# Kernel tuning notes

Measured on AMD Instinct MI355X. Metric: run time of the kernel, lower is better.

Reference implementation:

```python
import jax, jax.numpy as jnp
import numpy as np
from jax import lax

DN = ('NCDHW', 'OIDHW', 'NCDHW')


def dwconv(x, w, b):
    # depthwise 3D conv, 'same' padding (groups == channels of this branch)
    k = w.shape[-1]
    p = k // 2
    y = lax.conv_general_dilated(x, w, (1, 1, 1), [(p, p)] * 3,
                                 dimension_numbers=DN,
                                 feature_group_count=x.shape[1])
    return y + b[None, :, None, None, None]


def group_norm(x, w, b, groups=4, eps=1e-5):
    B, C, D, H, W = x.shape
    xr = x.reshape(B, groups, C // groups, D, H, W)
    mu = xr.mean(axis=(2, 3, 4, 5), keepdims=True)
    var = xr.var(axis=(2, 3, 4, 5), keepdims=True)
    xn = ((xr - mu) / jnp.sqrt(var + eps)).reshape(B, C, D, H, W)
    return xn * w[None, :, None, None, None] + b[None, :, None, None, None]


def instance_norm(x, eps=1e-5):
    # torch InstanceNorm3d default: affine=False, biased var, per (n,c) over spatial
    mu = x.mean(axis=(2, 3, 4), keepdims=True)
    var = x.var(axis=(2, 3, 4), keepdims=True)
    return (x - mu) / jnp.sqrt(var + eps)


def setup_inputs() -> dict:
    key = jax.random.key(0)
    B, C, D, H, W = 2, 32, 64, 64, 64
    gc = C // 4
    keys = jax.random.split(key, 12)
    inp = {"x": jax.random.normal(keys[0], (B, C, D, H, W), jnp.float32)}
    for i, k in enumerate([3, 5, 7, 9]):
        inp[f"w{k}"] = jax.random.normal(keys[1 + i], (gc, 1, k, k, k), jnp.float32) * (1.0 / k ** 1.5)
        inp[f"b{k}"] = jax.random.normal(keys[5 + i], (gc,), jnp.float32) * 0.01
    inp["gn_w"] = jnp.ones((C,), jnp.float32)
    inp["gn_b"] = jnp.zeros((C,), jnp.float32)
    inp["w_pw"] = jax.random.normal(keys[9], (gc, C), jnp.float32) * (1.0 / np.sqrt(C))
    inp["w_nxn"] = jax.random.normal(keys[10], (C, gc, 3, 3, 3), jnp.float32) * (1.0 / np.sqrt(gc * 27))
    return inp


def reference(x, w3, b3, w5, b5, w7, b7, w9, b9, gn_w, gn_b, w_pw, w_nxn):
    # split into 4 channel groups -> multi-kernel depthwise conv branches
    l, gs, gm, gl = jnp.split(x, 4, axis=1)
    y = jnp.concatenate([dwconv(l, w3, b3), dwconv(gs, w5, b5),
                         dwconv(gm, w7, b7), dwconv(gl, w9, b9)], axis=1) + x
    # GroupNorm(4) + exact GELU
    y = jax.nn.gelu(group_norm(y, gn_w, gn_b), approximate=False)
    # 1x1x1 conv (bias=False) + InstanceNorm + SiLU
    y = jax.nn.silu(instance_norm(jnp.einsum('bcdhw,oc->bodhw', y, w_pw)))
    # 3x3x3 conv (bias=False, pad 1) + InstanceNorm + SiLU
    y = lax.conv_general_dilated(y, w_nxn, (1, 1, 1), [(1, 1)] * 3, dimension_numbers=DN)
    y = jax.nn.silu(instance_norm(y))
    return y + x
```

## Files before the change

### kernel.cpp

```cpp
#include <hip/hip_runtime.h>
#include <cstddef>

#define SPATIAL (64*64*64)


__device__ __forceinline__ float wave_reduce(float v) {
    #pragma unroll
    for (int off = 32; off; off >>= 1) v += __shfl_down(v, off);
    return v;
}

__global__ void zero_stats(float* __restrict__ stats) {
    if (threadIdx.x < 176) stats[threadIdx.x] = 0.0f;
}


#define DW_RS    41
#define DW_SLICE (16 * DW_RS)

template<int K>
__device__ __forceinline__ void dw_impl(const float* __restrict__ x,
                                        const float* __restrict__ wsrc, float bias,
                                        int bc, int h0, int d0, int w0g,
                                        float* __restrict__ ls,
                                        float* __restrict__ stats, int b,
                                        float* __restrict__ y1)
{
    constexpr int P   = K / 2;
    constexpr int G   = P - 1;
    constexpr int WIN = 4 + 2 * P;
    constexpr int NS  = 16 + 2 * P;
    const float* xin = x + ((size_t)bc << 18);

    for (int i = threadIdx.x; i < NS * 640; i += 256) {
        const int zi  = i / 640;
        const int rem = i - zi * 640;
        const int row = rem / 40;
        const int col = rem - row * 40;
        const int zd = d0 - P + zi;
        const int zh = h0 - 4 + row;
        const int zw = w0g - 4 + col;
        float v = 0.0f;
        if (((unsigned)zd < 64u) & ((unsigned)zh < 64u) & ((unsigned)zw < 64u))
            v = xin[((size_t)zd << 12) + (zh << 6) + zw];
        ls[(zi + 4 - P) * DW_SLICE + row * DW_RS + col] = v;
    }
    __syncthreads();

    const int lane = threadIdx.x & 63;
    const int wave = threadIdx.x >> 6;
    const int wl   = lane & 7;
    const int r    = lane >> 3;
    const int dq   = d0 + (wave << 2);
    const int s0   = (wave << 2) + 4 - P;

    float acc[4][4];
    #pragma unroll
    for (int j = 0; j < 4; ++j)
        #pragma unroll
        for (int i = 0; i < 4; ++i) acc[j][i] = bias;

    for (int zq = 0; zq < K + 3; ++zq) {
        const float* sl = ls + (s0 + zq) * DW_SLICE;
        for (int kh = 0; kh < K; ++kh) {
            const float* rowp = sl + (r + kh + 4 - P) * DW_RS + ((wl << 2) + 4 - P);
            float win[WIN];
            #pragma unroll
            for (int t = 0; t < WIN; ++t) win[t] = rowp[t];
            #pragma unroll
            for (int j = 0; j < 4; ++j) {
                const int kd = zq - j;
                if (kd >= 0 && kd < K) {
                    const float* wr = wsrc + (kd * K + kh) * K;
                    #pragma unroll
                    for (int kw = 0; kw < K; ++kw) {
                        const float wt = wr[kw];
                        #pragma unroll
                        for (int i = 0; i < 4; ++i) acc[j][i] += win[kw + i] * wt;
                    }
                }
            }
        }
    }

    float gsum = 0.0f, gsq = 0.0f;
    #pragma unroll
    for (int j = 0; j < 4; ++j) {
        const float* cen = ls + ((wave << 2) + 4 + j) * DW_SLICE + (r + 4) * DW_RS + 4 + (wl << 2);
        #pragma unroll
        for (int i = 0; i < 4; ++i) acc[j][i] += cen[i];
        const size_t base = ((size_t)bc << 18) + ((size_t)(dq + j) << 12) +
                            ((size_t)(h0 + r) << 6) + (w0g + (wl << 2));
        *(float4*)(y1 + base) = make_float4(acc[j][0], acc[j][1], acc[j][2], acc[j][3]);
        #pragma unroll
        for (int i = 0; i < 4; ++i) { gsum += acc[j][i]; gsq += acc[j][i] * acc[j][i]; }
    }

    gsum = wave_reduce(gsum);
    gsq  = wave_reduce(gsq);
    if (lane == 0) {
        atomicAdd(&stats[b * 4 + G], gsum);
        atomicAdd(&stats[8 + b * 4 + G], gsq);
    }
}

__global__ __launch_bounds__(256) void dwconv_kernel(
    const float* __restrict__ x,
    const float* __restrict__ w3, const float* __restrict__ b3,
    const float* __restrict__ w5, const float* __restrict__ b5,
    const float* __restrict__ w7, const float* __restrict__ b7,
    const float* __restrict__ w9, const float* __restrict__ b9,
    float* __restrict__ y1, float* __restrict__ stats)
{
    __shared__ float ls[24 * DW_SLICE];
    const int gid = blockIdx.x;
    const int g   = 3 - (gid >> 10);
    const int rr  = gid & 1023;
    const int plane = rr >> 6;
    const int sub = rr & 63;
    const int hq  = sub >> 3;
    const int dc  = (sub >> 1) & 3;
    const int wc  = sub & 1;
    const int b   = plane >> 3, cl = plane & 7;
    const int bc  = (b << 5) + (g << 3) + cl;
    const int h0  = hq << 3, d0 = dc << 4, w0g = wc << 5;

    switch (g) {
        case 0: dw_impl<3>(x, w3 + cl * 27,  b3[cl], bc, h0, d0, w0g, ls, stats, b, y1); break;
        case 1: dw_impl<5>(x, w5 + cl * 125, b5[cl], bc, h0, d0, w0g, ls, stats, b, y1); break;
        case 2: dw_impl<7>(x, w7 + cl * 343, b7[cl], bc, h0, d0, w0g, ls, stats, b, y1); break;
        default: dw_impl<9>(x, w9 + cl * 729, b9[cl], bc, h0, d0, w0g, ls, stats, b, y1); break;
    }
}

__global__ void gn_finalize(const float* __restrict__ gn_w, const float* __restrict__ gn_b,
                            float* __restrict__ stats)
{
    const int i = threadIdx.x;
    if (i >= 64) return;
    const int b = i >> 5, c = i & 31, g = c >> 3;
    const float N = 8.0f * (float)SPATIAL;
    const float mu  = stats[b * 4 + g] / N;
    const float var = stats[8 + b * 4 + g] / N - mu * mu;
    const float rs  = rsqrtf(var + 1e-5f);
    const float a   = gn_w[c] * rs;
    stats[176 + i] = a;
    stats[240 + i] = gn_b[c] - mu * a;
}

__global__ __launch_bounds__(256) void pw_kernel(
    const float* __restrict__ y1, const float* __restrict__ w_pw,
    float* __restrict__ t, float* __restrict__ stats)
{
    const int bid = blockIdx.x;
    const int b   = bid >> 8;
    const int s   = (bid & 255) * 1024 + threadIdx.x * 4;

    const float* yb = y1 + ((size_t)b << 23);
    float acc[8][4] = {};

    for (int cc = 0; cc < 32; cc += 8) {
        float4 yv[8];
        #pragma unroll
        for (int u = 0; u < 8; ++u)
            yv[u] = *(const float4*)(yb + ((size_t)(cc + u) << 18) + s);
        #pragma unroll
        for (int u = 0; u < 8; ++u) {
            const int c = cc + u;
            const float ga = stats[176 + b * 32 + c];
            const float gs = stats[240 + b * 32 + c];
            float v0 = ga * yv[u].x + gs, v1 = ga * yv[u].y + gs;
            float v2 = ga * yv[u].z + gs, v3 = ga * yv[u].w + gs;
            const float e0 = 0.5f * v0 * (1.0f + erff(v0 * 0.70710678118654752f));
            const float e1 = 0.5f * v1 * (1.0f + erff(v1 * 0.70710678118654752f));
            const float e2 = 0.5f * v2 * (1.0f + erff(v2 * 0.70710678118654752f));
            const float e3 = 0.5f * v3 * (1.0f + erff(v3 * 0.70710678118654752f));
            #pragma unroll
            for (int o = 0; o < 8; ++o) {
                const float wt = w_pw[o * 32 + c];
                acc[o][0] += e0 * wt; acc[o][1] += e1 * wt;
                acc[o][2] += e2 * wt; acc[o][3] += e3 * wt;
            }
        }
    }

    float* tb = t + ((size_t)b << 21);
    #pragma unroll
    for (int o = 0; o < 8; ++o) {
        *(float4*)(tb + ((size_t)o << 18) + s) =
            make_float4(acc[o][0], acc[o][1], acc[o][2], acc[o][3]);
        float sm = acc[o][0] + acc[o][1] + acc[o][2] + acc[o][3];
        float sq = acc[o][0]*acc[o][0] + acc[o][1]*acc[o][1] +
                   acc[o][2]*acc[o][2] + acc[o][3]*acc[o][3];
        sm = wave_reduce(sm);
        sq = wave_reduce(sq);
        if ((threadIdx.x & 63) == 0) {
            atomicAdd(&stats[16 + b * 8 + o], sm);
            atomicAdd(&stats[32 + b * 8 + o], sq);
        }
    }
}

__global__ void in2_finalize(float* __restrict__ stats)
{
    const int i = threadIdx.x;
    if (i >= 16) return;
    const float N = (float)SPATIAL;
    const float mu  = stats[16 + i] / N;
    const float var = stats[32 + i] / N - mu * mu;
    stats[304 + i] = mu;
    stats[320 + i] = rsqrtf(var + 1e-5f);
}

#define C3_RS 41
#define C3_ROWSZ (10 * C3_RS)
#define C3_CH (3 * C3_ROWSZ)

__device__ __forceinline__ void c3_stage(const float* __restrict__ tb,
                                         float* __restrict__ ls,
                                         const float* __restrict__ stats,
                                         int b, int zd, int h0, int w0g)
{
    const bool dok = (unsigned)zd < 64u;
    const int slot = (zd + 33) % 3;
    for (int i = threadIdx.x; i < 8 * C3_ROWSZ; i += 256) {
        const int c   = i / C3_ROWSZ;
        const int rem = i - c * C3_ROWSZ;
        const int row = rem / C3_RS;
        const int col = rem - row * C3_RS;
        const int zh  = h0 - 1 + row;
        const int zw  = w0g + col - 4;
        float v = 0.0f;
        if (dok & ((unsigned)zh < 64u) & ((unsigned)zw < 64u)) {
            const float raw = tb[((size_t)c << 18) + ((size_t)zd << 12) + (zh << 6) + zw];
            const float mu = stats[304 + (b << 3) + c];
            const float rs = stats[320 + (b << 3) + c];
            const float xn = (raw - mu) * rs;
            v = xn / (1.0f + expf(-xn));
        }
        ls[c * C3_CH + slot * C3_ROWSZ + row * C3_RS + col] = v;
    }
}

__global__ __launch_bounds__(256) void conv3_kernel(
    const float* __restrict__ t, const float* __restrict__ w_nxn,
    float* __restrict__ out, float* __restrict__ stats)
{
    __shared__ float ls[8 * C3_CH];
    const int bid = blockIdx.x;
    const int b   = bid >> 8;
    const int r8  = bid & 255;
    const int d0  = (r8 >> 4) << 2;
    const int h0  = ((r8 >> 1) & 7) << 3;
    const int w0g = (r8 & 1) << 5;

    const int tid = threadIdx.x;
    const int w0  = (tid & 7) << 2;
    const int r   = (tid >> 3) & 7;
    const int oq  = __builtin_amdgcn_readfirstlane(tid >> 6);
    const int o0  = oq << 3;

    const float* tb = t + ((size_t)b << 21);
    float s3[8] = {}, q3[8] = {};

    c3_stage(tb, ls, stats, b, d0 - 1, h0, w0g);
    c3_stage(tb, ls, stats, b, d0,     h0, w0g);

    for (int d = d0; d < d0 + 4; ++d) {
        c3_stage(tb, ls, stats, b, d + 1, h0, w0g);
        __syncthreads();

        float acc[8][4] = {};
        for (int c = 0; c < 8; ++c) {
            const float* lc = ls + c * C3_CH;
            const float* wc = w_nxn + c * 27;
            #pragma unroll
            for (int kd = 0; kd < 3; ++kd) {
                const float* sl = lc + ((d + kd + 32) % 3) * C3_ROWSZ;
                #pragma unroll
                for (int kh = 0; kh < 3; ++kh) {
                    const float* rowp = sl + (r + kh) * C3_RS + w0 + 3;
                    float win[6];
                    #pragma unroll
                    for (int j = 0; j < 6; ++j) win[j] = rowp[j];
                    #pragma unroll
                    for (int oi = 0; oi < 8; ++oi) {
                        const float* wp = wc + (o0 + oi) * 216 + kd * 9 + kh * 3;
                        #pragma unroll
                        for (int kw = 0; kw < 3; ++kw) {
                            const float wt = wp[kw];
                            acc[oi][0] += win[kw]     * wt;
                            acc[oi][1] += win[kw + 1] * wt;
                            acc[oi][2] += win[kw + 2] * wt;
                            acc[oi][3] += win[kw + 3] * wt;
                        }
                    }
                }
            }
        }

        #pragma unroll
        for (int oi = 0; oi < 8; ++oi) {
            const int o = o0 + oi;
            *(float4*)(out + ((size_t)((b << 5) + o) << 18) + ((size_t)d << 12) +
                       ((size_t)(h0 + r) << 6) + (w0g + w0)) =
                make_float4(acc[oi][0], acc[oi][1], acc[oi][2], acc[oi][3]);
            s3[oi] += acc[oi][0] + acc[oi][1] + acc[oi][2] + acc[oi][3];
            q3[oi] += acc[oi][0]*acc[oi][0] + acc[oi][1]*acc[oi][1] +
                      acc[oi][2]*acc[oi][2] + acc[oi][3]*acc[oi][3];
        }
        __syncthreads();
    }

    #pragma unroll
    for (int oi = 0; oi < 8; ++oi) {
        float sm = wave_reduce(s3[oi]);
        float sq = wave_reduce(q3[oi]);
        if ((tid & 63) == 0) {
            atomicAdd(&stats[48 + (b << 5) + o0 + oi], sm);
            atomicAdd(&stats[112 + (b << 5) + o0 + oi], sq);
        }
    }
}

__global__ void in3_finalize(float* __restrict__ stats)
{
    const int i = threadIdx.x;
    if (i >= 64) return;
    const float N = (float)SPATIAL;
    const float mu  = stats[48 + i] / N;
    const float var = stats[112 + i] / N - mu * mu;
    stats[336 + i] = mu;
    stats[400 + i] = rsqrtf(var + 1e-5f);
}

__global__ __launch_bounds__(256) void final_kernel(
    const float* __restrict__ x, float* __restrict__ out, const float* __restrict__ stats)
{
    const int idx = blockIdx.x * 256 + threadIdx.x;
    const size_t i4 = (size_t)idx << 2;
    const int bc = (int)(i4 >> 18);
    const float mu = stats[336 + bc], rs = stats[400 + bc];
    float4 v = *(const float4*)(out + i4);
    const float4 xr = *(const float4*)(x + i4);
    v.x = (v.x - mu) * rs; v.x = v.x / (1.0f + expf(-v.x)) + xr.x;
    v.y = (v.y - mu) * rs; v.y = v.y / (1.0f + expf(-v.y)) + xr.y;
    v.z = (v.z - mu) * rs; v.z = v.z / (1.0f + expf(-v.z)) + xr.z;
    v.w = (v.w - mu) * rs; v.w = v.w / (1.0f + expf(-v.w)) + xr.w;
    *(float4*)(out + i4) = v;
}

extern "C" void kernel_launch(void* const* d_in, const int* in_sizes, int n_in,
                              void* d_out, int out_size, void* d_ws, size_t ws_size,
                              hipStream_t stream)
{
    const float* x    = (const float*)d_in[0];
    const float* w3   = (const float*)d_in[1];
    const float* b3   = (const float*)d_in[2];
    const float* w5   = (const float*)d_in[3];
    const float* b5   = (const float*)d_in[4];
    const float* w7   = (const float*)d_in[5];
    const float* b7   = (const float*)d_in[6];
    const float* w9   = (const float*)d_in[7];
    const float* b9   = (const float*)d_in[8];
    const float* gn_w = (const float*)d_in[9];
    const float* gn_b = (const float*)d_in[10];
    const float* w_pw = (const float*)d_in[11];
    const float* w_nxn= (const float*)d_in[12];

    char* ws = (char*)d_ws;
    float* t     = (float*)ws;
    float* stats = (float*)(ws + 16777216);

    float* out = (float*)d_out;

    zero_stats<<<1, 256, 0, stream>>>(stats);
    dwconv_kernel<<<4096, 256, 0, stream>>>(x, w3, b3, w5, b5, w7, b7, w9, b9, out, stats);
    gn_finalize<<<1, 64, 0, stream>>>(gn_w, gn_b, stats);
    pw_kernel<<<512, 256, 0, stream>>>(out, w_pw, t, stats);
    in2_finalize<<<1, 16, 0, stream>>>(stats);
    conv3_kernel<<<512, 256, 0, stream>>>(t, w_nxn, out, stats);
    in3_finalize<<<1, 64, 0, stream>>>(stats);
    final_kernel<<<16384, 256, 0, stream>>>(x, out, stats);
}
```

Before: 1.192 ms.

## Split depthwise conv per kernel size and stage conv3 weights in LDS

The single branchy depthwise-conv kernel is replaced by a templated kernel launched once per kernel size. Each block now handles 8 depth slices, 8 rows and 32 columns, with weights padded into LDS and float4 reads of both the input window and the weights. The 3x3x3 conv kernel stages all weights in LDS transposed by output channel and reads input rows with float4 loads over a narrower 36-float row. The aim is to cut scalar global weight loads and per-size shared-memory overprovisioning. The cost is four launches instead of one and a larger depth halo per output element.

```diff
diff --git a/kernel.cpp b/kernel.cpp
--- a/kernel.cpp
+++ b/kernel.cpp
@@ -15,121 +15,132 @@
 }
 
 
-#define DW_RS    41
-#define DW_SLICE (16 * DW_RS)
-
 template<int K>
-__device__ __forceinline__ void dw_impl(const float* __restrict__ x,
-                                        const float* __restrict__ wsrc, float bias,
-                                        int bc, int h0, int d0, int w0g,
-                                        float* __restrict__ ls,
-                                        float* __restrict__ stats, int b,
-                                        float* __restrict__ y1)
+__global__ __launch_bounds__(256) void dw_kernel(
+    const float* __restrict__ x, const float* __restrict__ wg,
+    const float* __restrict__ bg, float* __restrict__ y1, float* __restrict__ stats)
 {
     constexpr int P   = K / 2;
-    constexpr int G   = P - 1;
-    constexpr int WIN = 4 + 2 * P;
-    constexpr int NS  = 16 + 2 * P;
+    constexpr int G   = (K - 3) / 2;
+    constexpr int R   = 8 + 2 * P;
+    constexpr int NS  = 8 + 2 * P;
+    constexpr int CS  = 48;
+    constexpr int NZQ = K + 1;
+    constexpr int NF4 = (4 + 2 * P + 3) / 4;
+    constexpr int NW4 = (K + 3) / 4;
+
+    __shared__ float ls_x[NS * R * CS];
+    __shared__ float ls_w[K * K * 12];
+
+    const int gid   = blockIdx.x;
+    const int plane = gid >> 7;
+    const int sub   = gid & 127;
+    const int dc    = sub >> 4;
+    const int hq    = (sub >> 1) & 7;
+    const int wc    = sub & 1;
+    const int b     = plane >> 3, cl = plane & 7;
+    const int bc    = (b << 5) + (G << 3) + cl;
+    const int d0    = dc << 3, h0 = hq << 3, w0g = wc << 5;
+
     const float* xin = x + ((size_t)bc << 18);
-
-    for (int i = threadIdx.x; i < NS * 640; i += 256) {
-        const int zi  = i / 640;
-        const int rem = i - zi * 640;
-        const int row = rem / 40;
-        const int col = rem - row * 40;
-        const int zd = d0 - P + zi;
-        const int zh = h0 - 4 + row;
-        const int zw = w0g - 4 + col;
-        float v = 0.0f;
-        if (((unsigned)zd < 64u) & ((unsigned)zh < 64u) & ((unsigned)zw < 64u))
-            v = xin[((size_t)zd << 12) + (zh << 6) + zw];
-        ls[(zi + 4 - P) * DW_SLICE + row * DW_RS + col] = v;
+    const int tid = threadIdx.x;
+
+    for (int i = tid; i < K * K * 12; i += 256) {
+        const int kdkh = i / 12;
+        const int kw   = i - kdkh * 12;
+        ls_w[i] = (kw < K) ? wg[cl * K * K * K + kdkh * K + kw] : 0.0f;
+    }
+    for (int s = 0; s < NS; ++s) {
+        const int zd  = d0 - P + s;
+        const bool dok = (unsigned)zd < 64u;
+        float* dst = ls_x + s * (R * CS);
+        const float* src = xin + ((size_t)zd << 12);
+        for (int i = tid; i < R * CS; i += 256) {
+            const int row = i / CS;
+            const int col = i - row * CS;
+            const int zh = h0 - P + row;
+            const int zw = w0g - P + col;
+            float v = 0.0f;
+            if (dok & ((unsigned)zh < 64u) & ((unsigned)zw < 64u))
+                v = src[(zh << 6) + zw];
+            dst[i] = v;
+        }
     }
     __syncthreads();
 
-    const int lane = threadIdx.x & 63;
-    const int wave = threadIdx.x >> 6;
+    const int lane = tid & 63;
+    const int wave = tid >> 6;
+    const int r    = lane >> 3;
     const int wl   = lane & 7;
-    const int r    = lane >> 3;
-    const int dq   = d0 + (wave << 2);
-    const int s0   = (wave << 2) + 4 - P;
-
-    float acc[4][4];
+    const int u    = wave << 1;
+    const float bias = bg[cl];
+
+    float acc0[4], acc1[4];
     #pragma unroll
-    for (int j = 0; j < 4; ++j)
-        #pragma unroll
-        for (int i = 0; i < 4; ++i) acc[j][i] = bias;
-
-    for (int zq = 0; zq < K + 3; ++zq) {
-        const float* sl = ls + (s0 + zq) * DW_SLICE;
-        for (int kh = 0; kh < K; ++kh) {
-            const float* rowp = sl + (r + kh + 4 - P) * DW_RS + ((wl << 2) + 4 - P);
-            float win[WIN];
+    for (int i = 0; i < 4; ++i) { acc0[i] = bias; acc1[i] = bias; }
+
+    #pragma unroll 1
+    for (int kh = 0; kh < K; ++kh) {
+        const float* lsrow = ls_x + (r + kh) * CS + (wl << 2);
+        float wt[2][NW4 * 4];
+        #pragma unroll
+        for (int zq = 0; zq < NZQ; ++zq) {
+            if (zq < K) {
+                const float* wp = ls_w + (zq * K + kh) * 12;
+                #pragma unroll
+                for (int q = 0; q < NW4; ++q) {
+                    const float4 t = *(const float4*)(wp + 4 * q);
+                    wt[zq & 1][4*q+0] = t.x; wt[zq & 1][4*q+1] = t.y;
+                    wt[zq & 1][4*q+2] = t.z; wt[zq & 1][4*q+3] = t.w;
+                }
+            }
+            const float* rp = lsrow + (u + zq) * (R * CS);
+            float wn[NF4 * 4];
             #pragma unroll
-            for (int t = 0; t < WIN; ++t) win[t] = rowp[t];
-            #pragma unroll
-            for (int j = 0; j < 4; ++j) {
-                const int kd = zq - j;
-                if (kd >= 0 && kd < K) {
-                    const float* wr = wsrc + (kd * K + kh) * K;
+            for (int q = 0; q < NF4; ++q) {
+                const float4 t = *(const float4*)(rp + 4 * q);
+                wn[4*q+0] = t.x; wn[4*q+1] = t.y; wn[4*q+2] = t.z; wn[4*q+3] = t.w;
+            }
+            if (zq < K) {
+                #pragma unroll
+                for (int kw = 0; kw < K; ++kw) {
+                    const float w_ = wt[zq & 1][kw];
                     #pragma unroll
-                    for (int kw = 0; kw < K; ++kw) {
-                        const float wt = wr[kw];
-                        #pragma unroll
-                        for (int i = 0; i < 4; ++i) acc[j][i] += win[kw + i] * wt;
-                    }
+                    for (int i = 0; i < 4; ++i) acc0[i] += wn[kw + i] * w_;
                 }
             }
+            if (zq >= 1) {
+                #pragma unroll
+                for (int kw = 0; kw < K; ++kw) {
+                    const float w_ = wt[(zq + 1) & 1][kw];
+                    #pragma unroll
+                    for (int i = 0; i < 4; ++i) acc1[i] += wn[kw + i] * w_;
+                }
+            }
         }
     }
 
     float gsum = 0.0f, gsq = 0.0f;
-    #pragma unroll
-    for (int j = 0; j < 4; ++j) {
-        const float* cen = ls + ((wave << 2) + 4 + j) * DW_SLICE + (r + 4) * DW_RS + 4 + (wl << 2);
-        #pragma unroll
-        for (int i = 0; i < 4; ++i) acc[j][i] += cen[i];
-        const size_t base = ((size_t)bc << 18) + ((size_t)(dq + j) << 12) +
-                            ((size_t)(h0 + r) << 6) + (w0g + (wl << 2));
-        *(float4*)(y1 + base) = make_float4(acc[j][0], acc[j][1], acc[j][2], acc[j][3]);
-        #pragma unroll
-        for (int i = 0; i < 4; ++i) { gsum += acc[j][i]; gsq += acc[j][i] * acc[j][i]; }
-    }
-
+    {
+        const float* cen0 = ls_x + (u + P) * (R * CS) + (r + P) * CS + (wl << 2) + P;
+        const float* cen1 = cen0 + (R * CS);
+        #pragma unroll
+        for (int i = 0; i < 4; ++i) { acc0[i] += cen0[i]; acc1[i] += cen1[i]; }
+        const size_t base = ((size_t)bc << 18) + ((size_t)(d0 + u) << 12) +
+                            ((size_t)(h0 + r) << 6) + w0g + (wl << 2);
+        *(float4*)(y1 + base)          = make_float4(acc0[0], acc0[1], acc0[2], acc0[3]);
+        *(float4*)(y1 + base + 4096)   = make_float4(acc1[0], acc1[1], acc1[2], acc1[3]);
+        #pragma unroll
+        for (int i = 0; i < 4; ++i) {
+            gsum += acc0[i] + acc1[i];
+            gsq  += acc0[i]*acc0[i] + acc1[i]*acc1[i];
+        }
+    }
     gsum = wave_reduce(gsum);
     gsq  = wave_reduce(gsq);
     if (lane == 0) {
         atomicAdd(&stats[b * 4 + G], gsum);
         atomicAdd(&stats[8 + b * 4 + G], gsq);
-    }
-}
-
-__global__ __launch_bounds__(256) void dwconv_kernel(
-    const float* __restrict__ x,
-    const float* __restrict__ w3, const float* __restrict__ b3,
-    const float* __restrict__ w5, const float* __restrict__ b5,
-    const float* __restrict__ w7, const float* __restrict__ b7,
-    const float* __restrict__ w9, const float* __restrict__ b9,
-    float* __restrict__ y1, float* __restrict__ stats)
-{
-    __shared__ float ls[24 * DW_SLICE];
-    const int gid = blockIdx.x;
-    const int g   = 3 - (gid >> 10);
-    const int rr  = gid & 1023;
-    const int plane = rr >> 6;
-    const int sub = rr & 63;
-    const int hq  = sub >> 3;
-    const int dc  = (sub >> 1) & 3;
-    const int wc  = sub & 1;
-    const int b   = plane >> 3, cl = plane & 7;
-    const int bc  = (b << 5) + (g << 3) + cl;
-    const int h0  = hq << 3, d0 = dc << 4, w0g = wc << 5;
-
-    switch (g) {
-        case 0: dw_impl<3>(x, w3 + cl * 27,  b3[cl], bc, h0, d0, w0g, ls, stats, b, y1); break;
-        case 1: dw_impl<5>(x, w5 + cl * 125, b5[cl], bc, h0, d0, w0g, ls, stats, b, y1); break;
-        case 2: dw_impl<7>(x, w7 + cl * 343, b7[cl], bc, h0, d0, w0g, ls, stats, b, y1); break;
-        default: dw_impl<9>(x, w9 + cl * 729, b9[cl], bc, h0, d0, w0g, ls, stats, b, y1); break;
     }
 }
 
@@ -212,7 +223,7 @@
     stats[320 + i] = rsqrtf(var + 1e-5f);
 }
 
-#define C3_RS 41
+#define C3_RS 36
 #define C3_ROWSZ (10 * C3_RS)
 #define C3_CH (3 * C3_ROWSZ)
 
@@ -229,9 +240,9 @@
         const int row = rem / C3_RS;
         const int col = rem - row * C3_RS;
         const int zh  = h0 - 1 + row;
-        const int zw  = w0g + col - 4;
+        const int zw  = w0g + col - 1;
         float v = 0.0f;
-        if (dok & ((unsigned)zh < 64u) & ((unsigned)zw < 64u)) {
+        if (dok & ((unsigned)zh < 64u) & ((unsigned)zw < 64u) & (col < 34)) {
             const float raw = tb[((size_t)c << 18) + ((size_t)zd << 12) + (zh << 6) + zw];
             const float mu = stats[304 + (b << 3) + c];
             const float rs = stats[320 + (b << 3) + c];
@@ -247,6 +258,8 @@
     float* __restrict__ out, float* __restrict__ stats)
 {
     __shared__ float ls[8 * C3_CH];
+    __shared__ float lw[8 * 9 * 3 * 32];
+
     const int bid = blockIdx.x;
     const int b   = bid >> 8;
     const int r8  = bid & 255;
@@ -255,6 +268,15 @@
     const int w0g = (r8 & 1) << 5;
 
     const int tid = threadIdx.x;
+    for (int i = tid; i < 6912; i += 256) {
+        const int o    = i & 31;
+        const int rest = i >> 5;
+        const int kw   = rest % 3;
+        const int kdh  = (rest / 3) % 9;
+        const int c    = rest / 27;
+        lw[i] = w_nxn[o * 216 + c * 27 + kdh * 3 + kw];
+    }
+
     const int w0  = (tid & 7) << 2;
     const int r   = (tid >> 3) & 7;
     const int oq  = __builtin_amdgcn_readfirstlane(tid >> 6);
@@ -271,30 +293,36 @@
         __syncthreads();
 
         float acc[8][4] = {};
+        #pragma unroll 1
         for (int c = 0; c < 8; ++c) {
             const float* lc = ls + c * C3_CH;
-            const float* wc = w_nxn + c * 27;
             #pragma unroll
             for (int kd = 0; kd < 3; ++kd) {
                 const float* sl = lc + ((d + kd + 32) % 3) * C3_ROWSZ;
                 #pragma unroll
                 for (int kh = 0; kh < 3; ++kh) {
-                    const float* rowp = sl + (r + kh) * C3_RS + w0 + 3;
-                    float win[6];
+                    const float* rowp = sl + (r + kh) * C3_RS + w0;
+                    const float4 A = *(const float4*)rowp;
+                    const float4 B4 = *(const float4*)(rowp + 4);
+                    float wn[8] = {A.x, A.y, A.z, A.w, B4.x, B4.y, B4.z, B4.w};
+                    const float* wb = lw + ((c * 9 + kd * 3 + kh) * 3) * 32 + o0;
+                    float wt[3][8];
                     #pragma unroll
-                    for (int j = 0; j < 6; ++j) win[j] = rowp[j];
+                    for (int kw = 0; kw < 3; ++kw) {
+                        const float4 t0 = *(const float4*)(wb + kw * 32);
+                        const float4 t1 = *(const float4*)(wb + kw * 32 + 4);
+                        wt[kw][0]=t0.x; wt[kw][1]=t0.y; wt[kw][2]=t0.z; wt[kw][3]=t0.w;
+                        wt[kw][4]=t1.x; wt[kw][5]=t1.y; wt[kw][6]=t1.z; wt[kw][7]=t1.w;
+                    }
                     #pragma unroll
-                    for (int oi = 0; oi < 8; ++oi) {
-                        const float* wp = wc + (o0 + oi) * 216 + kd * 9 + kh * 3;
+                    for (int oi = 0; oi < 8; ++oi)
                         #pragma unroll
                         for (int kw = 0; kw < 3; ++kw) {
-                            const float wt = wp[kw];
-                            acc[oi][0] += win[kw]     * wt;
-                            acc[oi][1] += win[kw + 1] * wt;
-                            acc[oi][2] += win[kw + 2] * wt;
-                            acc[oi][3] += win[kw + 3] * wt;
+                            const float w_ = wt[kw][oi];
+                            #pragma unroll
+                            for (int i = 0; i < 4; ++i)
+                                acc[oi][i] += wn[kw + i] * w_;
                         }
-                    }
                 }
             }
         }
@@ -375,7 +403,10 @@
     float* out = (float*)d_out;
 
     zero_stats<<<1, 256, 0, stream>>>(stats);
-    dwconv_kernel<<<4096, 256, 0, stream>>>(x, w3, b3, w5, b5, w7, b7, w9, b9, out, stats);
+    dw_kernel<9><<<2048, 256, 0, stream>>>(x, w9, b9, out, stats);
+    dw_kernel<7><<<2048, 256, 0, stream>>>(x, w7, b7, out, stats);
+    dw_kernel<5><<<2048, 256, 0, stream>>>(x, w5, b5, out, stats);
+    dw_kernel<3><<<2048, 256, 0, stream>>>(x, w3, b3, out, stats);
     gn_finalize<<<1, 64, 0, stream>>>(gn_w, gn_b, stats);
     pw_kernel<<<512, 256, 0, stream>>>(out, w_pw, t, stats);
     in2_finalize<<<1, 16, 0, stream>>>(stats);
```

Measured after the change: 1.607 ms. 1.35x slower.
